# Performance work log

Measured on AMD Instinct MI355X. Metric: run time of the kernel, lower is better.

Reference implementation:

```python
import jax, jax.numpy as jnp
import numpy as np

H, D = 8, 8          # num_heads, hidden_size (head dim)
SCALE = 0.25         # Hopfield beta/scaling
STEPS = 3            # update_steps_max
LN_EPS = 1e-5


def ln(x, g, b):
    m = x.mean(-1, keepdims=True)
    v = ((x - m) ** 2).mean(-1, keepdims=True)
    return (x - m) * jax.lax.rsqrt(v + LN_EPS) * g + b


def setup_inputs() -> dict:
    key = jax.random.key(0)
    ks = jax.random.split(key, 8)
    B, N, E = 32, 512, 512
    P = H * D  # 64 virtual hopfield dim
    s = lambda k, shape: jax.random.normal(k, shape, jnp.float32) * 0.05
    return dict(
        x=jax.random.normal(ks[0], (B, N, E), jnp.float32),
        g_q=jnp.ones((E,), jnp.float32), b_q=jnp.zeros((E,), jnp.float32),
        g_k=jnp.ones((E,), jnp.float32), b_k=jnp.zeros((E,), jnp.float32),
        g_v=jnp.ones((E,), jnp.float32), b_v=jnp.zeros((E,), jnp.float32),
        Wq=s(ks[1], (P, E)), bq=jnp.zeros((P,), jnp.float32),
        Wk=s(ks[2], (P, E)), bk=jnp.zeros((P,), jnp.float32),
        Wv=s(ks[3], (P, E)), bv=jnp.zeros((P,), jnp.float32),
        Wo=s(ks[4], (E, P)), bo=jnp.zeros((E,), jnp.float32),
        Wl=s(ks[5], (1, N * E)), bl=jnp.zeros((1,), jnp.float32),
    )


def reference(x, g_q, b_q, g_k, b_k, g_v, b_v,
              Wq, bq, Wk, bk, Wv, bv, Wo, bo, Wl, bl):
    B, N, E = x.shape
    # LayerNorm on state (query), stored (key), projection (value) patterns
    q = (ln(x, g_q, b_q) @ Wq.T + bq).reshape(B, N, H, D)
    k = (ln(x, g_k, b_k) @ Wk.T + bk).reshape(B, N, H, D)
    v = (ln(x, g_v, b_v) @ Wv.T + bv).reshape(B, N, H, D)
    # iterative Hopfield retrieval: xi <- softmax(beta * xi K^T) K
    xi = q
    for _ in range(STEPS):
        a = jax.nn.softmax(SCALE * jnp.einsum('bihd,bjhd->bhij', xi, k), axis=-1)
        xi = jnp.einsum('bhij,bjhd->bihd', a, k)
    # final association with value patterns
    a = jax.nn.softmax(SCALE * jnp.einsum('bihd,bjhd->bhij', xi, k), axis=-1)
    o = jnp.einsum('bhij,bjhd->bihd', a, v).reshape(B, N, H * D)
    o = o @ Wo.T + bo              # (B, N, E) out projection
    y = o.reshape(B, N * E) @ Wl.T + bl  # (B, 1) classifier head
    return y.reshape(-1)           # flatten(start_dim=0) -> (B,)
```

## Files before the change

### kernel.cpp

```cpp
#include <hip/hip_runtime.h>

#define E_DIM 512
#define N_DIM 512
#define B_DIM 32
#define H_DIM 8
#define D_DIM 8
#define P3    192

typedef _Float16 half_t;
typedef __attribute__((ext_vector_type(2))) _Float16 half2v;
typedef __attribute__((ext_vector_type(4))) _Float16 half4v;
typedef __attribute__((ext_vector_type(8))) _Float16 half8v;
typedef __attribute__((ext_vector_type(4))) float f32x4;

#define PB_STRIDE 36
#define XS_STRIDE 520

__device__ inline float block_reduce_256(float v) {
    __shared__ float red[4];
    #pragma unroll
    for (int m = 32; m >= 1; m >>= 1) v += __shfl_xor(v, m);
    int w = threadIdx.x >> 6;
    if ((threadIdx.x & 63) == 0) red[w] = v;
    __syncthreads();
    if (threadIdx.x == 0) v = red[0] + red[1] + red[2] + red[3];
    return v;
}

__device__ inline half8v cvt8(float4 a, float4 b) {
    half8v h;
    h[0] = (half_t)a.x; h[1] = (half_t)a.y; h[2] = (half_t)a.z; h[3] = (half_t)a.w;
    h[4] = (half_t)b.x; h[5] = (half_t)b.y; h[6] = (half_t)b.z; h[7] = (half_t)b.w;
    return h;
}

__device__ inline half2v pk2(float a, float b) {
    return __builtin_bit_cast(half2v, __builtin_amdgcn_cvt_pkrtz(a, b));
}

__global__ __launch_bounds__(256) void prep_w(const float* __restrict__ Wq,
                        const float* __restrict__ Wk, const float* __restrict__ Wv,
                        const float* __restrict__ gq, const float* __restrict__ gk,
                        const float* __restrict__ gv,
                        const float* __restrict__ bnq, const float* __restrict__ bnk,
                        const float* __restrict__ bnv,
                        const float* __restrict__ bq, const float* __restrict__ bk,
                        const float* __restrict__ bv,
                        const float* __restrict__ bl,
                        half_t* __restrict__ WthF, float* __restrict__ colsum,
                        float* __restrict__ b2, float* __restrict__ y,
                        float* __restrict__ c0acc) {
    int pp = blockIdx.x;
    int which = pp >> 6, p = pp & 63;
    int ct = pp >> 4, c16 = pp & 15;
    const float* W  = (which == 0) ? Wq  : (which == 1) ? Wk  : Wv;
    const float* g  = (which == 0) ? gq  : (which == 1) ? gk  : gv;
    const float* bn = (which == 0) ? bnq : (which == 1) ? bnk : bnv;
    const float* bb = (which == 0) ? bq  : (which == 1) ? bk  : bv;
    int t = threadIdx.x;
    if (pp == 0) {
        if (t < 32) y[t] = bl[0];
        if (t == 32) c0acc[0] = 0.f;
    }
    float cs = 0.f, dt = 0.f;
    #pragma unroll
    for (int l = 0; l < 2; ++l) {
        int e = t + l * 256;
        float wv = W[p * E_DIM + e];
        half_t wh = (half_t)(wv * g[e]);
        int k32 = e >> 5, g2 = (e >> 3) & 3, j = e & 7;
        WthF[(((size_t)(ct * 16 + k32) * 64) + g2 * 16 + c16) * 8 + j] = wh;
        cs += (float)wh;
        dt += wv * bn[e];
    }
    cs = block_reduce_256(cs);
    __syncthreads();
    dt = block_reduce_256(dt);
    if (t == 0) { colsum[pp] = cs; b2[pp] = dt + bb[p]; }
}

__global__ __launch_bounds__(256) void ln_qkv_wl2(const float* __restrict__ x,
                                              const half_t* __restrict__ WthF,
                                              const float* __restrict__ b2,
                                              const float* __restrict__ colsum,
                                              half_t* __restrict__ qkv16,
                                              const float* __restrict__ Wl,
                                              const float* __restrict__ Wo,
                                              const float* __restrict__ bo,
                                              float* __restrict__ Wl2,
                                              float* __restrict__ c0acc) {
    __shared__ half_t Xs[16 * XS_STRIDE];
    __shared__ float stats[16][2];
    if (blockIdx.x < 1024) {
        const int t = threadIdx.x;
        const int lane = t & 63;
        const int w = t >> 6;
        const int g2 = lane >> 4, c16 = lane & 15;
        const int row0 = blockIdx.x * 16;
        {
            const int row = t >> 4, c = t & 15;
            const float4* xrow = (const float4*)(x + (size_t)(row0 + row) * E_DIM);
            float sx = 0.f, sxx = 0.f;
            #pragma unroll
            for (int l = 0; l < 8; ++l) {
                int f4 = c + l * 16;
                float4 a = xrow[f4];
                sx  += a.x + a.y + a.z + a.w;
                sxx += a.x*a.x + a.y*a.y + a.z*a.z + a.w*a.w;
                half4v h;
                h[0] = (half_t)a.x; h[1] = (half_t)a.y;
                h[2] = (half_t)a.z; h[3] = (half_t)a.w;
                *(half4v*)&Xs[row * XS_STRIDE + f4 * 4] = h;
            }
            #pragma unroll
            for (int m = 1; m <= 8; m <<= 1) {
                sx += __shfl_xor(sx, m); sxx += __shfl_xor(sxx, m);
            }
            if (c == 0) {
                float mean = sx * (1.f / E_DIM);
                float var  = sxx * (1.f / E_DIM) - mean * mean;
                stats[row][0] = mean;
                stats[row][1] = rsqrtf(var + 1e-5f);
            }
        }
        __syncthreads();
        f32x4 acc[3] = {{0.f,0.f,0.f,0.f},{0.f,0.f,0.f,0.f},{0.f,0.f,0.f,0.f}};
        const half_t* wf = WthF + (size_t)w * 3 * 16 * 512;
        #pragma unroll 4
        for (int k32 = 0; k32 < 16; ++k32) {
            half8v af = *(const half8v*)&Xs[c16 * XS_STRIDE + k32 * 32 + g2 * 8];
            #pragma unroll
            for (int nt = 0; nt < 3; ++nt) {
                half8v bf = *(const half8v*)(wf + ((size_t)(nt * 16 + k32)) * 512 + lane * 8);
                acc[nt] = __builtin_amdgcn_mfma_f32_16x16x32_f16(af, bf, acc[nt], 0, 0, 0);
            }
        }
        #pragma unroll
        for (int nt = 0; nt < 3; ++nt) {
            int pp = w * 48 + nt * 16 + c16;
            float cs = colsum[pp], bb = b2[pp];
            int which = pp >> 6, p = pp & 63;
            int h = p >> 3, d = p & 7;
            half_t* dst0 = qkv16 + (size_t)which * (B_DIM * H_DIM * N_DIM * D_DIM);
            #pragma unroll
            for (int r = 0; r < 4; ++r) {
                int rowi = g2 * 4 + r;
                float val = stats[rowi][1] * (acc[nt][r] - stats[rowi][0] * cs) + bb;
                int ng = row0 + rowi;
                int b = ng >> 9, n = ng & 511;
                dst0[(((size_t)(b * H_DIM + h)) * N_DIM + n) * D_DIM + d] = (half_t)val;
            }
        }
    } else {
        const int blk = blockIdx.x - 1024;
        const int t = threadIdx.x;
        const int lane = t & 63;
        const int w = t >> 6;
        const int g2 = lane >> 4, c16 = lane & 15;
        const int n0 = blk * 16;
        const int pcol = w * 16;
        f32x4 acc = {0.f, 0.f, 0.f, 0.f};
        float pc = 0.f;
        const float* arow = Wl + (size_t)(n0 + c16) * E_DIM;
        #pragma unroll 2
        for (int k0 = 0; k0 < E_DIM; k0 += 32) {
            int kbase = k0 + g2 * 8;
            float4 a0 = *(const float4*)(arow + kbase);
            float4 a1 = *(const float4*)(arow + kbase + 4);
            if (w == 0) {
                float4 b0 = *(const float4*)(bo + kbase);
                float4 b1 = *(const float4*)(bo + kbase + 4);
                pc += a0.x*b0.x + a0.y*b0.y + a0.z*b0.z + a0.w*b0.w
                    + a1.x*b1.x + a1.y*b1.y + a1.z*b1.z + a1.w*b1.w;
            }
            half8v af = cvt8(a0, a1);
            half8v bf;
            #pragma unroll
            for (int j = 0; j < 8; ++j)
                bf[j] = (half_t)Wo[(size_t)(kbase + j) * 64 + pcol + c16];
            acc = __builtin_amdgcn_mfma_f32_16x16x32_f16(af, bf, acc, 0, 0, 0);
        }
        int p = pcol + c16, h = p >> 3, d = p & 7;
        #pragma unroll
        for (int r = 0; r < 4; ++r) {
            int n = n0 + g2 * 4 + r;
            Wl2[h * (N_DIM * D_DIM) + n * D_DIM + d] = acc[r];
        }
        if (w == 0) {
            pc += __shfl_xor(pc, 16); pc += __shfl_xor(pc, 32);
            pc += __shfl_xor(pc, 1);  pc += __shfl_xor(pc, 2);
            pc += __shfl_xor(pc, 4);  pc += __shfl_xor(pc, 8);
            if (lane == 0) atomicAdd(c0acc, pc);
        }
    }
}

__global__ __launch_bounds__(256) void hopfield(const half_t* __restrict__ q16,
                                                const half_t* __restrict__ k16,
                                                const half_t* __restrict__ v16,
                                                const float* __restrict__ Wl2,
                                                const float* __restrict__ c0acc,
                                                float* __restrict__ y) {
    __shared__ half_t Kb[N_DIM * 8];
    __shared__ half_t Xi[128 * 8];
    __shared__ half_t KTb[16 * 536];
    __shared__ half_t Pb[4 * 16 * PB_STRIDE];
    const int t = threadIdx.x;
    const int lane = t & 63;
    const int w = t >> 6;
    const int g2 = lane >> 4;
    const int c16 = lane & 15;
    const int bh = blockIdx.x >> 2, seg = blockIdx.x & 3;
    const float C = 0.25f * 1.44269504088896f;
    const half_t* kg = k16 + (size_t)bh * (N_DIM * D_DIM);
    const half_t* vg = v16 + (size_t)bh * (N_DIM * D_DIM);
    const half_t* qg = q16 + (size_t)bh * (N_DIM * D_DIM) + seg * 128 * 8;
    const float* wl2p = Wl2 + (bh & 7) * (N_DIM * D_DIM) + seg * 128 * 8;

    for (int i = t; i < 536; i += 256) KTb[9 * 536 + i] = (half_t)0.f;
    {
        int j0 = 2 * t;
        half8v r0 = *(const half8v*)(kg + j0 * 8);
        half8v r1 = *(const half8v*)(kg + j0 * 8 + 8);
        *(half8v*)&Kb[j0 * 8] = r0;
        *(half8v*)&Kb[j0 * 8 + 8] = r1;
        #pragma unroll
        for (int d = 0; d < 8; ++d) {
            KTb[d * 536 + j0] = r0[d];
            KTb[d * 536 + j0 + 1] = r1[d];
        }
        KTb[8 * 536 + j0] = (half_t)1.f;
        KTb[8 * 536 + j0 + 1] = (half_t)1.f;
    }
    if (t < 128) {
        half8v hq = *(const half8v*)(qg + t * 8);
        half8v h;
        #pragma unroll
        for (int d = 0; d < 8; ++d) h[d] = (half_t)(C * (float)hq[d]);
        *(half8v*)&Xi[t * 8] = h;
    }
    __syncthreads();

    const half_t* zsrc = &KTb[9 * 536];
    half_t* myP = &Pb[w * 16 * PB_STRIDE];
    float fsum = 0.f;

    for (int it = 0; it < 4; ++it) {
        if (it == 3) {
            __syncthreads();
            int j0 = 2 * t;
            half8v r0 = *(const half8v*)(vg + j0 * 8);
            half8v r1 = *(const half8v*)(vg + j0 * 8 + 8);
            #pragma unroll
            for (int d = 0; d < 8; ++d) {
                KTb[d * 536 + j0] = r0[d];
                KTb[d * 536 + j0 + 1] = r1[d];
            }
            __syncthreads();
        }
        const half_t* x0p = (g2 == 0) ? &Xi[(w * 32 + c16) * 8] : zsrc;
        const half_t* x1p = (g2 == 0) ? &Xi[(w * 32 + 16 + c16) * 8] : zsrc;
        half8v bxi0 = *(const half8v*)x0p;
        half8v bxi1 = *(const half8v*)x1p;
        f32x4 U0 = {0.f, 0.f, 0.f, 0.f}, U1 = {0.f, 0.f, 0.f, 0.f};
        for (int j32 = 0; j32 < 16; ++j32) {
            half8v bKT = *(const half8v*)&KTb[c16 * 536 + j32 * 32 + g2 * 8];
            #pragma unroll
            for (int hh = 0; hh < 2; ++hh) {
                int jt16 = j32 * 2 + hh;
                const half_t* akp = (g2 == 0) ? &Kb[(jt16 * 16 + c16) * 8] : zsrc;
                half8v ak = *(const half8v*)akp;
                f32x4 S = {0.f, 0.f, 0.f, 0.f};
                S = __builtin_amdgcn_mfma_f32_16x16x32_f16(ak, bxi0, S, 0, 0, 0);
                half2v lo = pk2(__builtin_amdgcn_exp2f(S[0]), __builtin_amdgcn_exp2f(S[1]));
                half2v hi = pk2(__builtin_amdgcn_exp2f(S[2]), __builtin_amdgcn_exp2f(S[3]));
                half4v p = __builtin_shufflevector(lo, hi, 0, 1, 2, 3);
                *(half4v*)&myP[c16 * PB_STRIDE + hh * 16 + g2 * 4] = p;
            }
            {
                half4v alo = *(const half4v*)&myP[c16 * PB_STRIDE + g2 * 8];
                half4v ahi = *(const half4v*)&myP[c16 * PB_STRIDE + g2 * 8 + 4];
                half8v ap = __builtin_shufflevector(alo, ahi, 0, 1, 2, 3, 4, 5, 6, 7);
                U0 = __builtin_amdgcn_mfma_f32_16x16x32_f16(ap, bKT, U0, 0, 0, 0);
            }
            #pragma unroll
            for (int hh = 0; hh < 2; ++hh) {
                int jt16 = j32 * 2 + hh;
                const half_t* akp = (g2 == 0) ? &Kb[(jt16 * 16 + c16) * 8] : zsrc;
                half8v ak = *(const half8v*)akp;
                f32x4 S = {0.f, 0.f, 0.f, 0.f};
                S = __builtin_amdgcn_mfma_f32_16x16x32_f16(ak, bxi1, S, 0, 0, 0);
                half2v lo = pk2(__builtin_amdgcn_exp2f(S[0]), __builtin_amdgcn_exp2f(S[1]));
                half2v hi = pk2(__builtin_amdgcn_exp2f(S[2]), __builtin_amdgcn_exp2f(S[3]));
                half4v p = __builtin_shufflevector(lo, hi, 0, 1, 2, 3);
                *(half4v*)&myP[c16 * PB_STRIDE + hh * 16 + g2 * 4] = p;
            }
            {
                half4v alo = *(const half4v*)&myP[c16 * PB_STRIDE + g2 * 8];
                half4v ahi = *(const half4v*)&myP[c16 * PB_STRIDE + g2 * 8 + 4];
                half8v ap = __builtin_shufflevector(alo, ahi, 0, 1, 2, 3, 4, 5, 6, 7);
                U1 = __builtin_amdgcn_mfma_f32_16x16x32_f16(ap, bKT, U1, 0, 0, 0);
            }
        }
        int srcl = (lane & 48) | 8;
        #pragma unroll
        for (int r = 0; r < 4; ++r) {
            float l0 = __shfl(U0[r], srcl, 64);
            float l1 = __shfl(U1[r], srcl, 64);
            float inv0 = __builtin_amdgcn_rcpf(l0);
            float inv1 = __builtin_amdgcn_rcpf(l1);
            if (c16 < 8) {
                int i0 = w * 32 + g2 * 4 + r;
                int i1 = i0 + 16;
                if (it < 3) {
                    Xi[i0 * 8 + c16] = (half_t)(U0[r] * (C * inv0));
                    Xi[i1 * 8 + c16] = (half_t)(U1[r] * (C * inv1));
                } else {
                    fsum += (U0[r] * inv0) * wl2p[i0 * 8 + c16]
                          + (U1[r] * inv1) * wl2p[i1 * 8 + c16];
                }
            }
        }
    }
    float tot = block_reduce_256(fsum);
    if (t == 0) atomicAdd(&y[bh >> 3], tot);
    if (blockIdx.x == 0 && t < 32) {
        atomicAdd(&y[t], c0acc[0]);
    }
}

extern "C" void kernel_launch(void* const* d_in, const int* in_sizes, int n_in,
                              void* d_out, int out_size, void* d_ws, size_t ws_size,
                              hipStream_t stream) {
    const float* x   = (const float*)d_in[0];
    const float* g_q = (const float*)d_in[1];
    const float* b_q = (const float*)d_in[2];
    const float* g_k = (const float*)d_in[3];
    const float* b_k = (const float*)d_in[4];
    const float* g_v = (const float*)d_in[5];
    const float* b_v = (const float*)d_in[6];
    const float* Wq  = (const float*)d_in[7];
    const float* bq  = (const float*)d_in[8];
    const float* Wk  = (const float*)d_in[9];
    const float* bk  = (const float*)d_in[10];
    const float* Wv  = (const float*)d_in[11];
    const float* bv  = (const float*)d_in[12];
    const float* Wo  = (const float*)d_in[13];
    const float* bo  = (const float*)d_in[14];
    const float* Wl  = (const float*)d_in[15];
    const float* bl  = (const float*)d_in[16];
    float* out = (float*)d_out;

    float* ws = (float*)d_ws;
    float*  colsum = ws;
    float*  b2     = ws + 192;
    float*  c0acc  = ws + 384;
    float*  Wl2    = ws + 448;
    half_t* WthF   = (half_t*)(ws + 33216);
    half_t* qkv16  = (half_t*)(ws + 82368);

    half_t* q16 = qkv16;
    half_t* k16 = qkv16 + 1048576;
    half_t* v16 = qkv16 + 2097152;

    prep_w    <<<192, 256, 0, stream>>>(Wq, Wk, Wv, g_q, g_k, g_v,
                                        b_q, b_k, b_v, bq, bk, bv, bl,
                                        WthF, colsum, b2, out, c0acc);
    ln_qkv_wl2<<<1056, 256, 0, stream>>>(x, WthF, b2, colsum, qkv16,
                                         Wl, Wo, bo, Wl2, c0acc);
    hopfield  <<<1024, 256, 0, stream>>>(q16, k16, v16, Wl2, c0acc, out);
}
```

Measured before the change: 164.2 us.

## Emit MFMA-ready K/KT/VT layouts from projection and drop hopfield LDS staging

The projection kernel now writes K and the transposed K and V directly in MFMA fragment order, and extra blocks fill the rows of ones used for the softmax denominator. The hopfield kernel stops staging K/V into shared memory and reads fragments straight from global memory. It also halves the query rows per block so twice as many blocks launch, and raises the occupancy hint. This removes the LDS transpose and its barriers, in exchange for repeated global/L2 reads of K per wave and scattered 2-byte stores in the projection kernel.

```diff
diff --git a/kernel.cpp b/kernel.cpp
--- a/kernel.cpp
+++ b/kernel.cpp
@@ -83,7 +83,10 @@
                                               const half_t* __restrict__ WthF,
                                               const float* __restrict__ b2,
                                               const float* __restrict__ colsum,
-                                              half_t* __restrict__ qkv16,
+                                              half_t* __restrict__ q16,
+                                              half_t* __restrict__ KF,
+                                              half_t* __restrict__ KTF,
+                                              half_t* __restrict__ VTF,
                                               const float* __restrict__ Wl,
                                               const float* __restrict__ Wo,
                                               const float* __restrict__ bo,
@@ -141,17 +144,27 @@
             float cs = colsum[pp], bb = b2[pp];
             int which = pp >> 6, p = pp & 63;
             int h = p >> 3, d = p & 7;
-            half_t* dst0 = qkv16 + (size_t)which * (B_DIM * H_DIM * N_DIM * D_DIM);
             #pragma unroll
             for (int r = 0; r < 4; ++r) {
                 int rowi = g2 * 4 + r;
                 float val = stats[rowi][1] * (acc[nt][r] - stats[rowi][0] * cs) + bb;
                 int ng = row0 + rowi;
                 int b = ng >> 9, n = ng & 511;
-                dst0[(((size_t)(b * H_DIM + h)) * N_DIM + n) * D_DIM + d] = (half_t)val;
-            }
-        }
-    } else {
+                int bh = b * H_DIM + h;
+                half_t hv = (half_t)val;
+                if (which == 0) {
+                    q16[(((size_t)bh) * N_DIM + n) * D_DIM + d] = hv;
+                } else if (which == 1) {
+                    KF [((size_t)bh * 32 + (n >> 4)) * 128 + (n & 15) * 8 + d] = hv;
+                    KTF[((size_t)bh * 16 + (n >> 5)) * 512
+                        + (((n >> 3) & 3) * 16 + d) * 8 + (n & 7)] = hv;
+                } else {
+                    VTF[((size_t)bh * 16 + (n >> 5)) * 512
+                        + (((n >> 3) & 3) * 16 + d) * 8 + (n & 7)] = hv;
+                }
+            }
+        }
+    } else if (blockIdx.x < 1056) {
         const int blk = blockIdx.x - 1024;
         const int t = threadIdx.x;
         const int lane = t & 63;
@@ -192,132 +205,89 @@
             pc += __shfl_xor(pc, 4);  pc += __shfl_xor(pc, 8);
             if (lane == 0) atomicAdd(c0acc, pc);
         }
-    }
-}
-
-__global__ __launch_bounds__(256) void hopfield(const half_t* __restrict__ q16,
-                                                const half_t* __restrict__ k16,
-                                                const half_t* __restrict__ v16,
-                                                const float* __restrict__ Wl2,
-                                                const float* __restrict__ c0acc,
-                                                float* __restrict__ y) {
-    __shared__ half_t Kb[N_DIM * 8];
-    __shared__ half_t Xi[128 * 8];
-    __shared__ half_t KTb[16 * 536];
+    } else {
+        int tid = (blockIdx.x - 1056) * 256 + threadIdx.x;
+        half8v ones;
+        #pragma unroll
+        for (int j = 0; j < 8; ++j) ones[j] = (half_t)1.f;
+        for (int u = tid; u < 16384; u += 2048) {
+            int bh = u >> 6, rem = u & 63, j32 = rem >> 2, g2 = rem & 3;
+            size_t addr = ((size_t)(bh * 16 + j32)) * 512 + (g2 * 16 + 8) * 8;
+            *(half8v*)&KTF[addr] = ones;
+            *(half8v*)&VTF[addr] = ones;
+        }
+    }
+}
+
+__global__ __launch_bounds__(256, 8) void hopfield(const half_t* __restrict__ q16,
+                                                   const half_t* __restrict__ KF,
+                                                   const half_t* __restrict__ KTF,
+                                                   const half_t* __restrict__ VTF,
+                                                   const float* __restrict__ Wl2,
+                                                   const float* __restrict__ c0acc,
+                                                   float* __restrict__ y) {
+    __shared__ half_t Xi[64 * 8];
     __shared__ half_t Pb[4 * 16 * PB_STRIDE];
     const int t = threadIdx.x;
     const int lane = t & 63;
     const int w = t >> 6;
     const int g2 = lane >> 4;
     const int c16 = lane & 15;
-    const int bh = blockIdx.x >> 2, seg = blockIdx.x & 3;
+    const int bh = blockIdx.x & 255, seg = blockIdx.x >> 8;
     const float C = 0.25f * 1.44269504088896f;
-    const half_t* kg = k16 + (size_t)bh * (N_DIM * D_DIM);
-    const half_t* vg = v16 + (size_t)bh * (N_DIM * D_DIM);
-    const half_t* qg = q16 + (size_t)bh * (N_DIM * D_DIM) + seg * 128 * 8;
-    const float* wl2p = Wl2 + (bh & 7) * (N_DIM * D_DIM) + seg * 128 * 8;
-
-    for (int i = t; i < 536; i += 256) KTb[9 * 536 + i] = (half_t)0.f;
-    {
-        int j0 = 2 * t;
-        half8v r0 = *(const half8v*)(kg + j0 * 8);
-        half8v r1 = *(const half8v*)(kg + j0 * 8 + 8);
-        *(half8v*)&Kb[j0 * 8] = r0;
-        *(half8v*)&Kb[j0 * 8 + 8] = r1;
-        #pragma unroll
-        for (int d = 0; d < 8; ++d) {
-            KTb[d * 536 + j0] = r0[d];
-            KTb[d * 536 + j0 + 1] = r1[d];
-        }
-        KTb[8 * 536 + j0] = (half_t)1.f;
-        KTb[8 * 536 + j0 + 1] = (half_t)1.f;
-    }
-    if (t < 128) {
-        half8v hq = *(const half8v*)(qg + t * 8);
+    const half_t* qg  = q16 + ((size_t)bh * N_DIM + seg * 64) * D_DIM;
+    const half_t* kfb = KF  + (size_t)bh * 4096;
+    const half_t* ktb = KTF + (size_t)bh * 8192;
+    const half_t* vtb = VTF + (size_t)bh * 8192;
+    const float* wl2p = Wl2 + (bh & 7) * (N_DIM * D_DIM) + seg * 64 * 8;
+
+    if (lane < 16) {
+        half8v hq = *(const half8v*)(qg + (w * 16 + lane) * 8);
         half8v h;
         #pragma unroll
         for (int d = 0; d < 8; ++d) h[d] = (half_t)(C * (float)hq[d]);
-        *(half8v*)&Xi[t * 8] = h;
-    }
-    __syncthreads();
-
-    const half_t* zsrc = &KTb[9 * 536];
+        *(half8v*)&Xi[(w * 16 + lane) * 8] = h;
+    }
     half_t* myP = &Pb[w * 16 * PB_STRIDE];
     float fsum = 0.f;
 
+    #pragma unroll 1
     for (int it = 0; it < 4; ++it) {
-        if (it == 3) {
-            __syncthreads();
-            int j0 = 2 * t;
-            half8v r0 = *(const half8v*)(vg + j0 * 8);
-            half8v r1 = *(const half8v*)(vg + j0 * 8 + 8);
-            #pragma unroll
-            for (int d = 0; d < 8; ++d) {
-                KTb[d * 536 + j0] = r0[d];
-                KTb[d * 536 + j0 + 1] = r1[d];
-            }
-            __syncthreads();
-        }
-        const half_t* x0p = (g2 == 0) ? &Xi[(w * 32 + c16) * 8] : zsrc;
-        const half_t* x1p = (g2 == 0) ? &Xi[(w * 32 + 16 + c16) * 8] : zsrc;
-        half8v bxi0 = *(const half8v*)x0p;
-        half8v bxi1 = *(const half8v*)x1p;
-        f32x4 U0 = {0.f, 0.f, 0.f, 0.f}, U1 = {0.f, 0.f, 0.f, 0.f};
+        const half_t* btf = (it < 3) ? ktb : vtb;
+        half8v bxi = {};
+        if (g2 == 0) bxi = *(const half8v*)&Xi[(w * 16 + c16) * 8];
+        f32x4 U = {0.f, 0.f, 0.f, 0.f};
+        #pragma unroll 1
         for (int j32 = 0; j32 < 16; ++j32) {
-            half8v bKT = *(const half8v*)&KTb[c16 * 536 + j32 * 32 + g2 * 8];
+            half8v bKT = *(const half8v*)(btf + j32 * 512 + lane * 8);
             #pragma unroll
             for (int hh = 0; hh < 2; ++hh) {
                 int jt16 = j32 * 2 + hh;
-                const half_t* akp = (g2 == 0) ? &Kb[(jt16 * 16 + c16) * 8] : zsrc;
-                half8v ak = *(const half8v*)akp;
+                half8v ak = {};
+                if (g2 == 0) ak = *(const half8v*)(kfb + jt16 * 128 + c16 * 8);
                 f32x4 S = {0.f, 0.f, 0.f, 0.f};
-                S = __builtin_amdgcn_mfma_f32_16x16x32_f16(ak, bxi0, S, 0, 0, 0);
+                S = __builtin_amdgcn_mfma_f32_16x16x32_f16(ak, bxi, S, 0, 0, 0);
                 half2v lo = pk2(__builtin_amdgcn_exp2f(S[0]), __builtin_amdgcn_exp2f(S[1]));
                 half2v hi = pk2(__builtin_amdgcn_exp2f(S[2]), __builtin_amdgcn_exp2f(S[3]));
                 half4v p = __builtin_shufflevector(lo, hi, 0, 1, 2, 3);
                 *(half4v*)&myP[c16 * PB_STRIDE + hh * 16 + g2 * 4] = p;
             }
-            {
-                half4v alo = *(const half4v*)&myP[c16 * PB_STRIDE + g2 * 8];
-                half4v ahi = *(const half4v*)&myP[c16 * PB_STRIDE + g2 * 8 + 4];
-                half8v ap = __builtin_shufflevector(alo, ahi, 0, 1, 2, 3, 4, 5, 6, 7);
-                U0 = __builtin_amdgcn_mfma_f32_16x16x32_f16(ap, bKT, U0, 0, 0, 0);
-            }
-            #pragma unroll
-            for (int hh = 0; hh < 2; ++hh) {
-                int jt16 = j32 * 2 + hh;
-                const half_t* akp = (g2 == 0) ? &Kb[(jt16 * 16 + c16) * 8] : zsrc;
-                half8v ak = *(const half8v*)akp;
-                f32x4 S = {0.f, 0.f, 0.f, 0.f};
-                S = __builtin_amdgcn_mfma_f32_16x16x32_f16(ak, bxi1, S, 0, 0, 0);
-                half2v lo = pk2(__builtin_amdgcn_exp2f(S[0]), __builtin_amdgcn_exp2f(S[1]));
-                half2v hi = pk2(__builtin_amdgcn_exp2f(S[2]), __builtin_amdgcn_exp2f(S[3]));
-                half4v p = __builtin_shufflevector(lo, hi, 0, 1, 2, 3);
-                *(half4v*)&myP[c16 * PB_STRIDE + hh * 16 + g2 * 4] = p;
-            }
-            {
-                half4v alo = *(const half4v*)&myP[c16 * PB_STRIDE + g2 * 8];
-                half4v ahi = *(const half4v*)&myP[c16 * PB_STRIDE + g2 * 8 + 4];
-                half8v ap = __builtin_shufflevector(alo, ahi, 0, 1, 2, 3, 4, 5, 6, 7);
-                U1 = __builtin_amdgcn_mfma_f32_16x16x32_f16(ap, bKT, U1, 0, 0, 0);
-            }
+            half4v alo = *(const half4v*)&myP[c16 * PB_STRIDE + g2 * 8];
+            half4v ahi = *(const half4v*)&myP[c16 * PB_STRIDE + g2 * 8 + 4];
+            half8v ap = __builtin_shufflevector(alo, ahi, 0, 1, 2, 3, 4, 5, 6, 7);
+            U = __builtin_amdgcn_mfma_f32_16x16x32_f16(ap, bKT, U, 0, 0, 0);
         }
         int srcl = (lane & 48) | 8;
         #pragma unroll
         for (int r = 0; r < 4; ++r) {
-            float l0 = __shfl(U0[r], srcl, 64);
-            float l1 = __shfl(U1[r], srcl, 64);
-            float inv0 = __builtin_amdgcn_rcpf(l0);
-            float inv1 = __builtin_amdgcn_rcpf(l1);
+            float l0 = __shfl(U[r], srcl, 64);
+            float inv = __builtin_amdgcn_rcpf(l0);
             if (c16 < 8) {
-                int i0 = w * 32 + g2 * 4 + r;
-                int i1 = i0 + 16;
+                int i0 = w * 16 + g2 * 4 + r;
                 if (it < 3) {
-                    Xi[i0 * 8 + c16] = (half_t)(U0[r] * (C * inv0));
-                    Xi[i1 * 8 + c16] = (half_t)(U1[r] * (C * inv1));
+                    Xi[i0 * 8 + c16] = (half_t)(U[r] * (C * inv));
                 } else {
-                    fsum += (U0[r] * inv0) * wl2p[i0 * 8 + c16]
-                          + (U1[r] * inv1) * wl2p[i1 * 8 + c16];
+                    fsum += (U[r] * inv) * wl2p[i0 * 8 + c16];
                 }
             }
         }
@@ -357,16 +327,15 @@
     float*  c0acc  = ws + 384;
     float*  Wl2    = ws + 448;
     half_t* WthF   = (half_t*)(ws + 33216);
-    half_t* qkv16  = (half_t*)(ws + 82368);
-
-    half_t* q16 = qkv16;
-    half_t* k16 = qkv16 + 1048576;
-    half_t* v16 = qkv16 + 2097152;
+    half_t* q16    = (half_t*)(ws + 82368);
+    half_t* KF     = (half_t*)(ws + 606656);
+    half_t* KTF    = (half_t*)(ws + 1130944);
+    half_t* VTF    = (half_t*)(ws + 2179520);
 
     prep_w    <<<192, 256, 0, stream>>>(Wq, Wk, Wv, g_q, g_k, g_v,
                                         b_q, b_k, b_v, bq, bk, bv, bl,
                                         WthF, colsum, b2, out, c0acc);
-    ln_qkv_wl2<<<1056, 256, 0, stream>>>(x, WthF, b2, colsum, qkv16,
+    ln_qkv_wl2<<<1064, 256, 0, stream>>>(x, WthF, b2, colsum, q16, KF, KTF, VTF,
                                          Wl, Wo, bo, Wl2, c0acc);
-    hopfield  <<<1024, 256, 0, stream>>>(q16, k16, v16, Wl2, c0acc, out);
-}
+    hopfield  <<<2048, 256, 0, stream>>>(q16, KF, KTF, VTF, Wl2, c0acc, out);
+}
```

Measured after the change: 177.6 us. 1.08x slower.
